# Performance work log

Hardware: AMD Instinct MI355X
Metric: run time of the kernel (lower is better)

Reference implementation:

```python
import jax, jax.numpy as jnp
import numpy as np

B, T, C = 8, 1024, 1024   # batch, seq (== block_size), n_embed
H, D = 16, 64             # num_heads, head_size


def setup_inputs() -> dict:
    key = jax.random.key(0)
    kx, kq, kk, kv = jax.random.split(key, 4)
    scale = C ** -0.5  # mimic nn.Linear init scale roughly
    return {
        "x": jax.random.normal(kx, (B, T, C), dtype=jnp.float32),
        "Wq": jax.random.normal(kq, (H, C, D), dtype=jnp.float32) * scale,
        "Wk": jax.random.normal(kk, (H, C, D), dtype=jnp.float32) * scale,
        "Wv": jax.random.normal(kv, (H, C, D), dtype=jnp.float32) * scale,
    }


def reference(x, Wq, Wk, Wv):
    # Per-head Q/K/V projections (batched over heads instead of a Python loop)
    q = jnp.einsum("btc,hcd->bhtd", x, Wq)
    k = jnp.einsum("btc,hcd->bhtd", x, Wk)
    v = jnp.einsum("btc,hcd->bhtd", x, Wv)

    # scaled causal attention scores: [B, H, T, T]
    scores = jnp.einsum("bhtd,bhsd->bhts", q, k) * (D ** -0.5)
    causal = jnp.tril(jnp.ones((T, T), dtype=bool))
    scores = jnp.where(causal, scores, jnp.finfo(scores.dtype).min)
    attn = jax.nn.softmax(scores, axis=-1)

    out = jnp.einsum("bhts,bhsd->bhtd", attn, v)  # [B, H, T, D]
    # concat heads along last dim -> [B, T, H*D]
    return out.transpose(0, 2, 1, 3).reshape(B, T, H * D)
```

## Files before the change

### kernel.cpp

```cpp
#include <hip/hip_runtime.h>
#include <hip/hip_bf16.h>
#include <cstdint>


typedef __attribute__((ext_vector_type(8))) short short8;
typedef __attribute__((ext_vector_type(4))) short bfs4;
typedef __attribute__((ext_vector_type(4))) float f32x4;
typedef __attribute__((ext_vector_type(4))) int   i32x4;

__device__ __forceinline__ unsigned short f2bf(float f) {
  union { float f; unsigned int u; } v; v.f = f;
  unsigned int u = v.u;
  return (unsigned short)((u + 0x7fffu + ((u >> 16) & 1u)) >> 16);
}

__device__ __forceinline__ unsigned int pk_bf16(float a, float b) {
  union { __hip_bfloat162 h; unsigned int u; } cv;
  cv.h = __float22bfloat162_rn(make_float2(a, b));
  return cv.u;
}

__device__ __forceinline__ void gload_lds16(const void* g, void* l) {
  __builtin_amdgcn_global_load_lds(
      (const __attribute__((address_space(1))) void*)g,
      (__attribute__((address_space(3))) void*)l, 16, 0, 0);
}

__global__ __launch_bounds__(256) void k_convert(const float* __restrict__ x,
                                                 const float* __restrict__ Wq,
                                                 const float* __restrict__ Wk,
                                                 const float* __restrict__ Wv,
                                                 unsigned short* __restrict__ xb,
                                                 unsigned short* __restrict__ Wt) {
  const int bx = blockIdx.x;
  if (bx < 4096) {
    int g = bx * 256 + threadIdx.x;
    const float4* xp = (const float4*)x + (size_t)g * 2;
    float4 a = xp[0], b = xp[1];
    short8 o;
    o[0] = (short)f2bf(a.x); o[1] = (short)f2bf(a.y);
    o[2] = (short)f2bf(a.z); o[3] = (short)f2bf(a.w);
    o[4] = (short)f2bf(b.x); o[5] = (short)f2bf(b.y);
    o[6] = (short)f2bf(b.z); o[7] = (short)f2bf(b.w);
    *(short8*)(xb + (size_t)g * 8) = o;
  } else {
    int g = (bx - 4096) * 256 + threadIdx.x;
    int d  = g & 63;
    int cb = (g >> 6) & 127;
    int h  = (g >> 13) & 15;
    int p  = g >> 17;
    const float* W = (p == 0) ? Wq : (p == 1) ? Wk : Wv;
    const float* src = W + ((size_t)h * 1024 + cb * 8) * 64 + d;
    short8 o;
#pragma unroll
    for (int j = 0; j < 8; ++j) o[j] = (short)f2bf(src[(size_t)j * 64]);
    *(short8*)(Wt + (((size_t)p * 16 + h) * 64 + d) * 1024 + cb * 8) = o;
  }
}

__global__ __launch_bounds__(256, 2) void k_proj(const unsigned short* __restrict__ xb,
                                                 const unsigned short* __restrict__ Wt,
                                                 unsigned short* __restrict__ Qb,
                                                 unsigned short* __restrict__ Kb,
                                                 unsigned short* __restrict__ Vt) {
  __shared__ alignas(16) unsigned short As[3][8192];
  __shared__ alignas(16) unsigned short Bs[3][4096];
  const int p   = blockIdx.y;
  const int bx  = blockIdx.x;
  const int tid = threadIdx.x;
  const int lane = tid & 63, w = tid >> 6;
  const int ln = lane & 15, quad = lane >> 4;
  const int wm = w >> 1, wn = w & 1;

  const unsigned short* Abase;
  const unsigned short* Bbase;
  int m0, n0;
  const int c = bx & 7, j = bx >> 3;
  if (p < 2) {
    Abase = xb; Bbase = Wt + (size_t)p * 1048576;
    m0 = ((j & 3) * 8 + c) * 256;
    n0 = (j >> 2) * 128;
  } else {
    Abase = Wt + (size_t)2 * 1048576; Bbase = xb;
    m0 = (j >> 3) * 256;
    n0 = ((j & 7) * 8 + c) * 128;
  }

  auto stage = [&](int t, int buf) {
    const int c0 = t * 32;
#pragma unroll
    for (int jj = 0; jj < 4; ++jj) {
      int cch = jj * 256 + tid;
      int iln = cch & 15, iq = (cch >> 4) & 3, mb = cch >> 6;
      gload_lds16(Abase + (size_t)(m0 + mb * 16 + iln) * 1024 + c0 + iq * 8,
                  (char*)&As[buf][0] + (size_t)(jj * 256 + w * 64) * 16);
    }
#pragma unroll
    for (int jj = 0; jj < 2; ++jj) {
      int cch = jj * 256 + tid;
      int iln = cch & 15, iq = (cch >> 4) & 3, nb = cch >> 6;
      gload_lds16(Bbase + (size_t)(n0 + nb * 16 + iln) * 1024 + c0 + iq * 8,
                  (char*)&Bs[buf][0] + (size_t)(jj * 256 + w * 64) * 16);
    }
  };

  f32x4 acc[8][4];
#pragma unroll
  for (int i = 0; i < 8; ++i)
#pragma unroll
    for (int jj = 0; jj < 4; ++jj) acc[i][jj] = (f32x4){0.f, 0.f, 0.f, 0.f};

  stage(0, 0);
  stage(1, 1);
  asm volatile("s_waitcnt vmcnt(6)" ::: "memory");
  __builtin_amdgcn_s_barrier();

  int rb = 0;
  for (int t = 0; t < 32; ++t) {
    int sb = rb + 2; if (sb >= 3) sb -= 3;
    if (t <= 29) stage(t + 2, sb);

    short8 af[8], bfv[4];
#pragma unroll
    for (int m = 0; m < 8; ++m)
      af[m] = *(const short8*)&As[rb][(size_t)((wm * 8 + m) * 64 + quad * 16 + ln) * 8];
#pragma unroll
    for (int n = 0; n < 4; ++n)
      bfv[n] = *(const short8*)&Bs[rb][(size_t)((wn * 4 + n) * 64 + quad * 16 + ln) * 8];

#pragma unroll
    for (int m = 0; m < 8; ++m)
#pragma unroll
      for (int n = 0; n < 4; ++n)
        acc[m][n] = __builtin_amdgcn_mfma_f32_16x16x32_bf16(
            af[m], bfv[n], acc[m][n], 0, 0, 0);

    if (t < 30) {
      asm volatile("s_waitcnt vmcnt(6)" ::: "memory");
      __builtin_amdgcn_s_barrier();
    } else if (t == 30) {
      asm volatile("s_waitcnt vmcnt(0)" ::: "memory");
      __builtin_amdgcn_s_barrier();
    }
    if (++rb == 3) rb = 0;
  }

  unsigned short* outp = (p == 0) ? Qb : (p == 1) ? Kb : Vt;
#pragma unroll
  for (int mt = 0; mt < 8; ++mt)
#pragma unroll
    for (int nt = 0; nt < 4; ++nt)
#pragma unroll
      for (int r = 0; r < 4; ++r) {
        int m = m0 + wm * 128 + mt * 16 + quad * 4 + r;
        int n = n0 + wn * 64 + nt * 16 + ln;
        size_t addr;
        if (p < 2) {
          addr = ((size_t)(m >> 10) * 16 + (n >> 6)) * 65536 + (size_t)(m & 1023) * 64 + (n & 63);
        } else {
          addr = ((size_t)(n >> 10) * 1024 + m) * 1024 + (n & 1023);
        }
        outp[addr] = f2bf(acc[mt][nt][r]);
      }
}

__global__ __launch_bounds__(256) void k_attn(const unsigned short* __restrict__ Qb,
                                              const unsigned short* __restrict__ Kb,
                                              const unsigned short* __restrict__ Vt,
                                              float* __restrict__ out) {
  __shared__ alignas(16) unsigned short Ks[4096];
  __shared__ alignas(16) unsigned short Vs[4096];
  __shared__ alignas(16) unsigned short Ps[8192];
  const int bid = blockIdx.x;
  const int qb = 7 - (bid >> 7);
  const int bh = bid & 127;
  const int b = bh >> 4, h = bh & 15;
  const int tid = threadIdx.x, lane = tid & 63, w = tid >> 6;
  const int ln = lane & 15, quad = lane >> 4;

  i32x4 rk[2], rv[2];
  auto ldkv = [&](int kt) {
    const int s0 = kt * 64;
#pragma unroll
    for (int i = 0; i < 2; ++i) {
      int idx = i * 256 + tid;
      int iln = idx & 15, iq = (idx >> 4) & 3, ikk = (idx >> 6) & 1, it = (idx >> 7) & 3;
      rk[i] = *(const i32x4*)(Kb + ((size_t)bh * 1024 + s0 + it * 16 + iln) * 64 + ikk * 32 + iq * 8);
      rv[i] = *(const i32x4*)(Vt + ((size_t)bh * 64 + it * 16 + iln) * 1024 + s0 + ikk * 32 + iq * 8);
    }
  };

  short8 qf[2][2];
#pragma unroll
  for (int qt = 0; qt < 2; ++qt) {
    const int q = qb * 128 + qt * 64 + w * 16 + ln;
#pragma unroll
    for (int kk = 0; kk < 2; ++kk)
      qf[qt][kk] = *(const short8*)(Qb + ((size_t)bh * 1024 + q) * 64 + kk * 32 + quad * 8);
  }

  f32x4 o[2][4];
#pragma unroll
  for (int qt = 0; qt < 2; ++qt)
#pragma unroll
    for (int dt = 0; dt < 4; ++dt) o[qt][dt] = (f32x4){0.f, 0.f, 0.f, 0.f};
  float l_i[2] = {0.f, 0.f};
  const float sc = 0.18033688011112042f;
  const float FM = 16.0f;

  const int ktmax = 2 * qb + 1;
  ldkv(0);

  for (int kt = 0; kt <= ktmax; ++kt) {
    const int s0 = kt * 64;
#pragma unroll
    for (int i = 0; i < 2; ++i) {
      *(i32x4*)((char*)Ks + (size_t)(i * 256 + tid) * 16) = rk[i];
      *(i32x4*)((char*)Vs + (size_t)(i * 256 + tid) * 16) = rv[i];
    }
    __syncthreads();
    if (kt < ktmax) ldkv(kt + 1);

    f32x4 st[2][4];
    __builtin_amdgcn_s_setprio(1);
#pragma unroll
    for (int s = 0; s < 4; ++s) {
      st[0][s] = (f32x4){0.f, 0.f, 0.f, 0.f};
      st[1][s] = (f32x4){0.f, 0.f, 0.f, 0.f};
#pragma unroll
      for (int kk = 0; kk < 2; ++kk) {
        short8 kf = *(const short8*)&Ks[(size_t)(((s * 2 + kk) * 4 + quad) * 16 + ln) * 8];
        st[0][s] = __builtin_amdgcn_mfma_f32_16x16x32_bf16(kf, qf[0][kk], st[0][s], 0, 0, 0);
        st[1][s] = __builtin_amdgcn_mfma_f32_16x16x32_bf16(kf, qf[1][kk], st[1][s], 0, 0, 0);
      }
    }
    __builtin_amdgcn_s_setprio(0);

#pragma unroll
    for (int qt = 0; qt < 2; ++qt) {
      const int q = qb * 128 + qt * 64 + w * 16 + ln;
      const bool masked = (kt >= 2 * qb + qt);
      float pv[4][4];
      float rs = 0.f;
#pragma unroll
      for (int s = 0; s < 4; ++s)
#pragma unroll
        for (int r = 0; r < 4; ++r) {
          float v = fmaf(st[qt][s][r], sc, -FM);
          if (masked) {
            int sidx = s0 + s * 16 + quad * 4 + r;
            if (sidx > q) v = -1.0e30f;
          }
          float e = __builtin_amdgcn_exp2f(v);
          pv[s][r] = e;
          rs += e;
        }
      rs += __shfl_xor(rs, 16);
      rs += __shfl_xor(rs, 32);
      l_i[qt] += rs;

      unsigned short* Pq = Ps + (w * 2 + qt) * 1024;
#pragma unroll
      for (int s = 0; s < 4; ++s) {
        union { bfs4 v; unsigned int u[2]; } pk;
        pk.u[0] = pk_bf16(pv[s][0], pv[s][1]);
        pk.u[1] = pk_bf16(pv[s][2], pv[s][3]);
        *(bfs4*)&Pq[(s * 2 + (quad >> 1)) * 128 + ln * 8 + (quad & 1) * 4] = pk.v;
      }
    }

    __builtin_amdgcn_s_setprio(1);
#pragma unroll
    for (int kk = 0; kk < 2; ++kk) {
      short8 pf0 = *(const short8*)&Ps[(size_t)(w * 2 + 0) * 1024 + (size_t)((kk * 4 + quad) * 16 + ln) * 8];
      short8 pf1 = *(const short8*)&Ps[(size_t)(w * 2 + 1) * 1024 + (size_t)((kk * 4 + quad) * 16 + ln) * 8];
#pragma unroll
      for (int dt = 0; dt < 4; ++dt) {
        short8 vf = *(const short8*)&Vs[(size_t)(((dt * 2 + kk) * 4 + quad) * 16 + ln) * 8];
        o[0][dt] = __builtin_amdgcn_mfma_f32_16x16x32_bf16(vf, pf0, o[0][dt], 0, 0, 0);
        o[1][dt] = __builtin_amdgcn_mfma_f32_16x16x32_bf16(vf, pf1, o[1][dt], 0, 0, 0);
      }
    }
    __builtin_amdgcn_s_setprio(0);

    __syncthreads();
  }

#pragma unroll
  for (int qt = 0; qt < 2; ++qt) {
    const int q = qb * 128 + qt * 64 + w * 16 + ln;
    const float rl = 1.0f / l_i[qt];
#pragma unroll
    for (int dt = 0; dt < 4; ++dt) {
      float4 ov;
      ov.x = o[qt][dt][0] * rl; ov.y = o[qt][dt][1] * rl;
      ov.z = o[qt][dt][2] * rl; ov.w = o[qt][dt][3] * rl;
      *(float4*)(out + ((size_t)b * 1024 + q) * 1024 + h * 64 + dt * 16 + quad * 4) = ov;
    }
  }
}

extern "C" void kernel_launch(void* const* d_in, const int* in_sizes, int n_in,
                              void* d_out, int out_size, void* d_ws, size_t ws_size,
                              hipStream_t stream) {
  const float* x  = (const float*)d_in[0];
  const float* Wq = (const float*)d_in[1];
  const float* Wk = (const float*)d_in[2];
  const float* Wv = (const float*)d_in[3];
  float* out = (float*)d_out;

  unsigned short* ws = (unsigned short*)d_ws;
  unsigned short* xb = ws;
  unsigned short* Wt = ws + 8388608;
  unsigned short* Qb = ws + 11534336;
  unsigned short* Kb = ws + 19922944;
  unsigned short* Vt = ws + 28311552;

  hipLaunchKernelGGL(k_convert, dim3(5632), dim3(256), 0, stream, x, Wq, Wk, Wv, xb, Wt);
  hipLaunchKernelGGL(k_proj, dim3(256, 3), dim3(256), 0, stream, xb, Wt, Qb, Kb, Vt);
  hipLaunchKernelGGL(k_attn, dim3(1024), dim3(256), 0, stream, Qb, Kb, Vt, out);
}
```

Measured before the change: 227.0 us.

## Widen attention blocks to 256 queries with 8 waves sharing K/V tiles

The attention kernel now runs 512 threads per block, and each block covers 256 query rows instead of 128, so the grid halves to 512 blocks. Each K/V tile staged in shared memory is reused by twice as many waves, which cuts global K/V loads and the per-thread staging work. The query-row mapping and the causal mask condition are reorganized so each wave owns 32 contiguous rows. The setprio hints are removed. In exchange there are fewer blocks for the causal load imbalance to spread across, and larger shared-memory and thread-count demands per block that may reduce occupancy.

```diff
diff --git a/kernel.cpp b/kernel.cpp
--- a/kernel.cpp
+++ b/kernel.cpp
@@ -164,36 +164,32 @@
       }
 }
 
-__global__ __launch_bounds__(256) void k_attn(const unsigned short* __restrict__ Qb,
+__global__ __launch_bounds__(512) void k_attn(const unsigned short* __restrict__ Qb,
                                               const unsigned short* __restrict__ Kb,
                                               const unsigned short* __restrict__ Vt,
                                               float* __restrict__ out) {
   __shared__ alignas(16) unsigned short Ks[4096];
   __shared__ alignas(16) unsigned short Vs[4096];
-  __shared__ alignas(16) unsigned short Ps[8192];
+  __shared__ alignas(16) unsigned short Ps[16384];
   const int bid = blockIdx.x;
-  const int qb = 7 - (bid >> 7);
+  const int qb = 3 - (bid >> 7);
   const int bh = bid & 127;
   const int b = bh >> 4, h = bh & 15;
   const int tid = threadIdx.x, lane = tid & 63, w = tid >> 6;
   const int ln = lane & 15, quad = lane >> 4;
 
-  i32x4 rk[2], rv[2];
+  i32x4 rk, rv;
   auto ldkv = [&](int kt) {
     const int s0 = kt * 64;
-#pragma unroll
-    for (int i = 0; i < 2; ++i) {
-      int idx = i * 256 + tid;
-      int iln = idx & 15, iq = (idx >> 4) & 3, ikk = (idx >> 6) & 1, it = (idx >> 7) & 3;
-      rk[i] = *(const i32x4*)(Kb + ((size_t)bh * 1024 + s0 + it * 16 + iln) * 64 + ikk * 32 + iq * 8);
-      rv[i] = *(const i32x4*)(Vt + ((size_t)bh * 64 + it * 16 + iln) * 1024 + s0 + ikk * 32 + iq * 8);
-    }
+    int iln = tid & 15, iq = (tid >> 4) & 3, ikk = (tid >> 6) & 1, it = (tid >> 7) & 3;
+    rk = *(const i32x4*)(Kb + ((size_t)bh * 1024 + s0 + it * 16 + iln) * 64 + ikk * 32 + iq * 8);
+    rv = *(const i32x4*)(Vt + ((size_t)bh * 64 + it * 16 + iln) * 1024 + s0 + ikk * 32 + iq * 8);
   };
 
   short8 qf[2][2];
 #pragma unroll
   for (int qt = 0; qt < 2; ++qt) {
-    const int q = qb * 128 + qt * 64 + w * 16 + ln;
+    const int q = qb * 256 + w * 32 + qt * 16 + ln;
 #pragma unroll
     for (int kk = 0; kk < 2; ++kk)
       qf[qt][kk] = *(const short8*)(Qb + ((size_t)bh * 1024 + q) * 64 + kk * 32 + quad * 8);
@@ -208,21 +204,17 @@
   const float sc = 0.18033688011112042f;
   const float FM = 16.0f;
 
-  const int ktmax = 2 * qb + 1;
+  const int ktmax = 4 * qb + 3;
   ldkv(0);
 
   for (int kt = 0; kt <= ktmax; ++kt) {
     const int s0 = kt * 64;
-#pragma unroll
-    for (int i = 0; i < 2; ++i) {
-      *(i32x4*)((char*)Ks + (size_t)(i * 256 + tid) * 16) = rk[i];
-      *(i32x4*)((char*)Vs + (size_t)(i * 256 + tid) * 16) = rv[i];
-    }
+    *(i32x4*)((char*)Ks + (size_t)tid * 16) = rk;
+    *(i32x4*)((char*)Vs + (size_t)tid * 16) = rv;
     __syncthreads();
     if (kt < ktmax) ldkv(kt + 1);
 
     f32x4 st[2][4];
-    __builtin_amdgcn_s_setprio(1);
 #pragma unroll
     for (int s = 0; s < 4; ++s) {
       st[0][s] = (f32x4){0.f, 0.f, 0.f, 0.f};
@@ -234,12 +226,12 @@
         st[1][s] = __builtin_amdgcn_mfma_f32_16x16x32_bf16(kf, qf[1][kk], st[1][s], 0, 0, 0);
       }
     }
-    __builtin_amdgcn_s_setprio(0);
 
 #pragma unroll
     for (int qt = 0; qt < 2; ++qt) {
-      const int q = qb * 128 + qt * 64 + w * 16 + ln;
-      const bool masked = (kt >= 2 * qb + qt);
+      const int qbase = qb * 256 + w * 32 + qt * 16;
+      const int q = qbase + ln;
+      const bool masked = (kt >= (qbase >> 6));
       float pv[4][4];
       float rs = 0.f;
 #pragma unroll
@@ -269,7 +261,6 @@
       }
     }
 
-    __builtin_amdgcn_s_setprio(1);
 #pragma unroll
     for (int kk = 0; kk < 2; ++kk) {
       short8 pf0 = *(const short8*)&Ps[(size_t)(w * 2 + 0) * 1024 + (size_t)((kk * 4 + quad) * 16 + ln) * 8];
@@ -281,14 +272,13 @@
         o[1][dt] = __builtin_amdgcn_mfma_f32_16x16x32_bf16(vf, pf1, o[1][dt], 0, 0, 0);
       }
     }
-    __builtin_amdgcn_s_setprio(0);
 
     __syncthreads();
   }
 
 #pragma unroll
   for (int qt = 0; qt < 2; ++qt) {
-    const int q = qb * 128 + qt * 64 + w * 16 + ln;
+    const int q = qb * 256 + w * 32 + qt * 16 + ln;
     const float rl = 1.0f / l_i[qt];
 #pragma unroll
     for (int dt = 0; dt < 4; ++dt) {
@@ -318,5 +308,5 @@
 
   hipLaunchKernelGGL(k_convert, dim3(5632), dim3(256), 0, stream, x, Wq, Wk, Wv, xb, Wt);
   hipLaunchKernelGGL(k_proj, dim3(256, 3), dim3(256), 0, stream, xb, Wt, Qb, Kb, Vt);
-  hipLaunchKernelGGL(k_attn, dim3(1024), dim3(256), 0, stream, Qb, Kb, Vt, out);
-}
+  hipLaunchKernelGGL(k_attn, dim3(512), dim3(512), 0, stream, Qb, Kb, Vt, out);
+}
```

New measurement: 237.3 us. 4.5% more time.

## Shrink projection GEMM to single-wave 128x64 tiles with double buffering

Applied to the files above, without the earlier changes.

The projection GEMM moves from 256-thread blocks computing 256x128 tiles with a triple-buffered pipeline to single-wave blocks computing 128x64 tiles with a double buffer. Because each block is one wave, the workgroup barriers go away and grid size grows fourfold, which gives more blocks per CU to hide latency. The cost is less operand reuse per block, so total global and L2 traffic rises, and the loop waits for each load with vmcnt(0). Separately, the s_setprio priority hints are removed from the attention kernel.

```diff
diff --git a/kernel.cpp b/kernel.cpp
--- a/kernel.cpp
+++ b/kernel.cpp
@@ -58,19 +58,17 @@
   }
 }
 
-__global__ __launch_bounds__(256, 2) void k_proj(const unsigned short* __restrict__ xb,
-                                                 const unsigned short* __restrict__ Wt,
-                                                 unsigned short* __restrict__ Qb,
-                                                 unsigned short* __restrict__ Kb,
-                                                 unsigned short* __restrict__ Vt) {
-  __shared__ alignas(16) unsigned short As[3][8192];
-  __shared__ alignas(16) unsigned short Bs[3][4096];
-  const int p   = blockIdx.y;
-  const int bx  = blockIdx.x;
-  const int tid = threadIdx.x;
-  const int lane = tid & 63, w = tid >> 6;
+__global__ __launch_bounds__(64) void k_proj(const unsigned short* __restrict__ xb,
+                                             const unsigned short* __restrict__ Wt,
+                                             unsigned short* __restrict__ Qb,
+                                             unsigned short* __restrict__ Kb,
+                                             unsigned short* __restrict__ Vt) {
+  __shared__ alignas(16) unsigned short As[2][4096];
+  __shared__ alignas(16) unsigned short Bs[2][2048];
+  const int p    = blockIdx.y;
+  const int bx   = blockIdx.x;
+  const int lane = threadIdx.x;
   const int ln = lane & 15, quad = lane >> 4;
-  const int wm = w >> 1, wn = w & 1;
 
   const unsigned short* Abase;
   const unsigned short* Bbase;
@@ -78,30 +76,24 @@
   const int c = bx & 7, j = bx >> 3;
   if (p < 2) {
     Abase = xb; Bbase = Wt + (size_t)p * 1048576;
-    m0 = ((j & 3) * 8 + c) * 256;
-    n0 = (j >> 2) * 128;
+    m0 = ((j & 7) * 8 + c) * 128;
+    n0 = (j >> 3) * 64;
   } else {
     Abase = Wt + (size_t)2 * 1048576; Bbase = xb;
-    m0 = (j >> 3) * 256;
-    n0 = ((j & 7) * 8 + c) * 128;
+    m0 = (j >> 4) * 128;
+    n0 = ((j & 15) * 8 + c) * 64;
   }
 
   auto stage = [&](int t, int buf) {
-    const int c0 = t * 32;
-#pragma unroll
-    for (int jj = 0; jj < 4; ++jj) {
-      int cch = jj * 256 + tid;
-      int iln = cch & 15, iq = (cch >> 4) & 3, mb = cch >> 6;
-      gload_lds16(Abase + (size_t)(m0 + mb * 16 + iln) * 1024 + c0 + iq * 8,
-                  (char*)&As[buf][0] + (size_t)(jj * 256 + w * 64) * 16);
-    }
-#pragma unroll
-    for (int jj = 0; jj < 2; ++jj) {
-      int cch = jj * 256 + tid;
-      int iln = cch & 15, iq = (cch >> 4) & 3, nb = cch >> 6;
-      gload_lds16(Bbase + (size_t)(n0 + nb * 16 + iln) * 1024 + c0 + iq * 8,
-                  (char*)&Bs[buf][0] + (size_t)(jj * 256 + w * 64) * 16);
-    }
+    const int col = t * 32 + quad * 8;
+    const unsigned short* arow = Abase + (size_t)(m0 + ln) * 1024 + col;
+    const unsigned short* brow = Bbase + (size_t)(n0 + ln) * 1024 + col;
+#pragma unroll
+    for (int i = 0; i < 8; ++i)
+      gload_lds16(arow + (size_t)i * 16 * 1024, (char*)&As[buf][0] + (size_t)i * 1024);
+#pragma unroll
+    for (int i = 0; i < 4; ++i)
+      gload_lds16(brow + (size_t)i * 16 * 1024, (char*)&Bs[buf][0] + (size_t)i * 1024);
   };
 
   f32x4 acc[8][4];
@@ -111,22 +103,19 @@
     for (int jj = 0; jj < 4; ++jj) acc[i][jj] = (f32x4){0.f, 0.f, 0.f, 0.f};
 
   stage(0, 0);
-  stage(1, 1);
-  asm volatile("s_waitcnt vmcnt(6)" ::: "memory");
-  __builtin_amdgcn_s_barrier();
-
-  int rb = 0;
+  asm volatile("s_waitcnt vmcnt(0)" ::: "memory");
+
+  int buf = 0;
   for (int t = 0; t < 32; ++t) {
-    int sb = rb + 2; if (sb >= 3) sb -= 3;
-    if (t <= 29) stage(t + 2, sb);
+    if (t < 31) stage(t + 1, buf ^ 1);
 
     short8 af[8], bfv[4];
 #pragma unroll
     for (int m = 0; m < 8; ++m)
-      af[m] = *(const short8*)&As[rb][(size_t)((wm * 8 + m) * 64 + quad * 16 + ln) * 8];
+      af[m] = *(const short8*)&As[buf][(size_t)((m * 4 + quad) * 16 + ln) * 8];
 #pragma unroll
     for (int n = 0; n < 4; ++n)
-      bfv[n] = *(const short8*)&Bs[rb][(size_t)((wn * 4 + n) * 64 + quad * 16 + ln) * 8];
+      bfv[n] = *(const short8*)&Bs[buf][(size_t)((n * 4 + quad) * 16 + ln) * 8];
 
 #pragma unroll
     for (int m = 0; m < 8; ++m)
@@ -135,14 +124,8 @@
         acc[m][n] = __builtin_amdgcn_mfma_f32_16x16x32_bf16(
             af[m], bfv[n], acc[m][n], 0, 0, 0);
 
-    if (t < 30) {
-      asm volatile("s_waitcnt vmcnt(6)" ::: "memory");
-      __builtin_amdgcn_s_barrier();
-    } else if (t == 30) {
-      asm volatile("s_waitcnt vmcnt(0)" ::: "memory");
-      __builtin_amdgcn_s_barrier();
-    }
-    if (++rb == 3) rb = 0;
+    asm volatile("s_waitcnt vmcnt(0)" ::: "memory");
+    buf ^= 1;
   }
 
   unsigned short* outp = (p == 0) ? Qb : (p == 1) ? Kb : Vt;
@@ -152,8 +135,8 @@
     for (int nt = 0; nt < 4; ++nt)
 #pragma unroll
       for (int r = 0; r < 4; ++r) {
-        int m = m0 + wm * 128 + mt * 16 + quad * 4 + r;
-        int n = n0 + wn * 64 + nt * 16 + ln;
+        int m = m0 + mt * 16 + quad * 4 + r;
+        int n = n0 + nt * 16 + ln;
         size_t addr;
         if (p < 2) {
           addr = ((size_t)(m >> 10) * 16 + (n >> 6)) * 65536 + (size_t)(m & 1023) * 64 + (n & 63);
@@ -222,7 +205,6 @@
     if (kt < ktmax) ldkv(kt + 1);
 
     f32x4 st[2][4];
-    __builtin_amdgcn_s_setprio(1);
 #pragma unroll
     for (int s = 0; s < 4; ++s) {
       st[0][s] = (f32x4){0.f, 0.f, 0.f, 0.f};
@@ -234,7 +216,6 @@
         st[1][s] = __builtin_amdgcn_mfma_f32_16x16x32_bf16(kf, qf[1][kk], st[1][s], 0, 0, 0);
       }
     }
-    __builtin_amdgcn_s_setprio(0);
 
 #pragma unroll
     for (int qt = 0; qt < 2; ++qt) {
@@ -269,7 +250,6 @@
       }
     }
 
-    __builtin_amdgcn_s_setprio(1);
 #pragma unroll
     for (int kk = 0; kk < 2; ++kk) {
       short8 pf0 = *(const short8*)&Ps[(size_t)(w * 2 + 0) * 1024 + (size_t)((kk * 4 + quad) * 16 + ln) * 8];
@@ -281,7 +261,6 @@
         o[1][dt] = __builtin_amdgcn_mfma_f32_16x16x32_bf16(vf, pf1, o[1][dt], 0, 0, 0);
       }
     }
-    __builtin_amdgcn_s_setprio(0);
 
     __syncthreads();
   }
@@ -317,6 +296,6 @@
   unsigned short* Vt = ws + 28311552;
 
   hipLaunchKernelGGL(k_convert, dim3(5632), dim3(256), 0, stream, x, Wq, Wk, Wv, xb, Wt);
-  hipLaunchKernelGGL(k_proj, dim3(256, 3), dim3(256), 0, stream, xb, Wt, Qb, Kb, Vt);
+  hipLaunchKernelGGL(k_proj, dim3(1024, 3), dim3(64), 0, stream, xb, Wt, Qb, Kb, Vt);
   hipLaunchKernelGGL(k_attn, dim3(1024), dim3(256), 0, stream, Qb, Kb, Vt, out);
 }
```

New measurement: 274.0 us. 1.21x slower.
